# Kernel tuning notes

Hardware: AMD Instinct MI355X
Metric: run time of the kernel (lower is better)

Reference implementation:

```python
import jax, jax.numpy as jnp
import numpy as np

DIM = 768
GP_NUM = 49


def setup_inputs() -> dict:
    key = jax.random.key(0)
    ks = jax.random.split(key, 7)
    b, n, d = 16, 1024, DIM
    s = d ** -0.5
    x = jax.random.normal(ks[0], (b, n, d), dtype=jnp.float32)
    W_qkv = jax.random.normal(ks[1], (d, 3 * d), dtype=jnp.float32) * s
    b_qkv = jnp.zeros((3 * d,), dtype=jnp.float32)
    W_proj = jax.random.normal(ks[2], (d, d), dtype=jnp.float32) * s
    b_proj = jnp.zeros((d,), dtype=jnp.float32)
    W_gp = jax.random.normal(ks[3], (d, GP_NUM), dtype=jnp.float32) * s
    alpha = jnp.zeros((1,), dtype=jnp.float32)
    return {"x": x, "W_qkv": W_qkv, "b_qkv": b_qkv, "W_proj": W_proj,
            "b_proj": b_proj, "W_gp": W_gp, "alpha": alpha}


def reference(x, W_qkv, b_qkv, W_proj, b_proj, W_gp, alpha):
    d = x.shape[-1]
    scale = d ** -0.5
    qkv = x @ W_qkv + b_qkv                      # (b, n, 3d)
    q, k, v = jnp.split(qkv, 3, axis=-1)
    scores = jnp.einsum('bnd,bmd->bnm', q, k) * scale
    attn = jax.nn.softmax(scores, axis=-1)       # (b, n, n)
    gw = jax.nn.softmax(q @ W_gp, axis=-1)       # (b, n, gp_num)
    group = jnp.einsum('bng,bmg->bnm', gw, gw)   # (b, n, n)
    a = jax.nn.sigmoid(alpha)                    # (1,)
    weights = attn * (a + (1.0 - a) * group)
    out = jnp.einsum('bnm,bmd->bnd', weights, v)
    return out @ W_proj + b_proj
```

## Files before the change

### kernel.cpp

```cpp
#include <hip/hip_runtime.h>
#include <stdint.h>

typedef __attribute__((ext_vector_type(8))) short short8;
typedef __attribute__((ext_vector_type(4))) short short4v;
typedef __attribute__((ext_vector_type(4))) float floatx4;
typedef _Float16 half2v __attribute__((ext_vector_type(2)));

__device__ __forceinline__ float b2f(unsigned short u) {
  union { unsigned int i; float f; } v; v.i = ((unsigned int)u) << 16; return v.f;
}
__device__ __forceinline__ unsigned short f2b(float f) {
  union { float f; unsigned int i; } v; v.f = f;
  unsigned int i = v.i;
  return (unsigned short)((i + 0x7FFFu + ((i >> 16) & 1u)) >> 16);
}
__device__ __forceinline__ short4v pack4(float a, float b, float c, float d) {
  short4v r;
  r[0] = (short)f2b(a); r[1] = (short)f2b(b); r[2] = (short)f2b(c); r[3] = (short)f2b(d);
  return r;
}

__device__ __forceinline__ void stage16(const unsigned short* g, unsigned short* lds_base) {
  __builtin_amdgcn_global_load_lds((__attribute__((address_space(1))) const unsigned int*)g,
                                   (__attribute__((address_space(3))) unsigned int*)lds_base,
                                   16, 0, 0);
}

template<int SWZ>
__global__ __launch_bounds__(256, 4) void gemm_bt(
    const unsigned short* __restrict__ A, const unsigned short* __restrict__ B,
    unsigned short* __restrict__ Cb, float* __restrict__ Cf,
    const float* __restrict__ rowdiv, const float* __restrict__ bias,
    int K, int lda, int ldb, int ldc,
    long long sA, long long sB, long long sC, long long sRD)
{
  const int tid  = threadIdx.x;
  const int lane = tid & 63;
  const int wave = tid >> 6;
  const int wr = wave >> 1, wc = wave & 1;
  int m0, n0;
  if (SWZ) {
    const int lin  = blockIdx.x;
    const int xcd  = lin & 7;
    const int rem  = lin >> 3;
    const int yloc = rem / 18;
    const int x    = rem - yloc * 18;
    m0 = (xcd * 16 + yloc) * 128;
    n0 = x * 128;
  } else {
    m0 = blockIdx.y * 128;
    n0 = blockIdx.x * 128;
  }
  const int bz = blockIdx.z;
  A += (long long)bz * sA;
  B += (long long)bz * sB;
  const float* rd = rowdiv ? rowdiv + (long long)bz * sRD : (const float*)0;

  __shared__ unsigned short As[128 * 32];
  __shared__ unsigned short Bs[128 * 32];

  floatx4 acc[4][4];
#pragma unroll
  for (int i = 0; i < 4; ++i)
#pragma unroll
    for (int j = 0; j < 4; ++j) acc[i][j] = floatx4{0.f, 0.f, 0.f, 0.f};

  const int t    = (lane & 7) ^ (lane >> 3);
  const int srow = 2 * (lane >> 3) + (t >> 2);
  const int scol = (t & 3) * 8;
  const unsigned short* ga0 = A + (long long)(m0 + wave * 32 + srow) * lda + scol;
  const unsigned short* ga1 = ga0 + 16LL * lda;
  const unsigned short* gb0 = B + (long long)(n0 + wave * 32 + srow) * ldb + scol;
  const unsigned short* gb1 = gb0 + 16LL * ldb;
  unsigned short* lA0 = As + wave * 1024;
  unsigned short* lA1 = lA0 + 512;
  unsigned short* lB0 = Bs + wave * 1024;
  unsigned short* lB1 = lB0 + 512;

  const int l15  = lane & 15;
  const int q    = lane >> 4;
  const int rofs = (l15 >> 1) * 64 + (((q + 4 * (l15 & 1)) ^ (l15 >> 1)) * 8);

  for (int kt = 0; kt < K; kt += 32) {
    __syncthreads();
    stage16(ga0 + kt, lA0);
    stage16(ga1 + kt, lA1);
    stage16(gb0 + kt, lB0);
    stage16(gb1 + kt, lB1);
    __syncthreads();
    short8 af[4], bfv[4];
#pragma unroll
    for (int i = 0; i < 4; ++i) af[i]  = *(const short8*)&As[(wr * 32 + i * 8) * 64 + rofs];
#pragma unroll
    for (int j = 0; j < 4; ++j) bfv[j] = *(const short8*)&Bs[(wc * 32 + j * 8) * 64 + rofs];
#pragma unroll
    for (int i = 0; i < 4; ++i)
#pragma unroll
      for (int j = 0; j < 4; ++j)
        acc[i][j] = __builtin_amdgcn_mfma_f32_16x16x32_bf16(bfv[j], af[i], acc[i][j], 0, 0, 0);
  }

#pragma unroll
  for (int i = 0; i < 4; ++i) {
    const int row = m0 + wr * 64 + i * 16 + l15;
    const float rcp = rd ? __builtin_amdgcn_rcpf(rd[row]) : 1.0f;
#pragma unroll
    for (int j = 0; j < 4; ++j) {
      const int colb = n0 + wc * 64 + j * 16 + q * 4;
      floatx4 v = acc[i][j];
      if (rd) { v[0] *= rcp; v[1] *= rcp; v[2] *= rcp; v[3] *= rcp; }
      if (bias) {
        const float4 bi = *(const float4*)&bias[colb];
        v[0] += bi.x; v[1] += bi.y; v[2] += bi.z; v[3] += bi.w;
      }
      if (Cb) *(short4v*)&Cb[(long long)bz * sC + (long long)row * ldc + colb] = pack4(v[0], v[1], v[2], v[3]);
      else    *(floatx4*)&Cf[(long long)bz * sC + (long long)row * ldc + colb] = v;
    }
  }
}

__global__ __launch_bounds__(256) void score_weights(
    const unsigned short* __restrict__ qkv, const unsigned short* __restrict__ gw,
    unsigned short* __restrict__ Wout, float* __restrict__ L,
    const float* __restrict__ alpha)
{
  const int tid  = threadIdx.x;
  const int lane = tid & 63;
  const int wave = tid >> 6;
  const int wr = wave >> 1, wc = wave & 1;
  const int n0 = blockIdx.x * 128;
  const int m0 = blockIdx.y * 128;
  const int b  = blockIdx.z;

  const int l15 = lane & 15;
  const int q   = lane >> 4;
  const int q8  = q * 8;

  const unsigned short* gq = gw + ((long long)(b * 1024 + m0 + wr * 64)) * 64;
  const unsigned short* gk = gw + ((long long)(b * 1024 + n0 + wc * 64)) * 64;
  floatx4 gacc[4][4];
#pragma unroll
  for (int i = 0; i < 4; ++i)
#pragma unroll
    for (int j = 0; j < 4; ++j) gacc[i][j] = floatx4{0.f, 0.f, 0.f, 0.f};
#pragma unroll
  for (int ks = 0; ks < 2; ++ks) {
    short8 af[4], bfv[4];
#pragma unroll
    for (int i = 0; i < 4; ++i) af[i]  = *(const short8*)&gq[(long long)(i * 16 + l15) * 64 + ks * 32 + q8];
#pragma unroll
    for (int j = 0; j < 4; ++j) bfv[j] = *(const short8*)&gk[(long long)(j * 16 + l15) * 64 + ks * 32 + q8];
#pragma unroll
    for (int i = 0; i < 4; ++i)
#pragma unroll
      for (int j = 0; j < 4; ++j)
        gacc[i][j] = __builtin_amdgcn_mfma_f32_16x16x32_bf16(bfv[j], af[i], gacc[i][j], 0, 0, 0);
  }
  const float aa    = 1.0f / (1.0f + __expf(-alpha[0]));
  const float onema = 1.0f - aa;
  half2v gfp[4][4][2];
#pragma unroll
  for (int i = 0; i < 4; ++i)
#pragma unroll
    for (int j = 0; j < 4; ++j) {
      gfp[i][j][0] = half2v{(_Float16)(aa + onema * gacc[i][j][0]),
                            (_Float16)(aa + onema * gacc[i][j][1])};
      gfp[i][j][1] = half2v{(_Float16)(aa + onema * gacc[i][j][2]),
                            (_Float16)(aa + onema * gacc[i][j][3])};
    }

  const unsigned short* Aq = qkv + ((long long)(b * 1024 + m0)) * 2304;
  const unsigned short* Bk = qkv + ((long long)(b * 1024 + n0)) * 2304 + 768;

  __shared__ unsigned short As[128 * 32];
  __shared__ unsigned short Bs[128 * 32];

  floatx4 sacc[4][4];
#pragma unroll
  for (int i = 0; i < 4; ++i)
#pragma unroll
    for (int j = 0; j < 4; ++j) sacc[i][j] = floatx4{0.f, 0.f, 0.f, 0.f};

  const int t    = (lane & 7) ^ (lane >> 3);
  const int srow = 2 * (lane >> 3) + (t >> 2);
  const int scol = (t & 3) * 8;
  const unsigned short* ga0 = Aq + (long long)(wave * 32 + srow) * 2304 + scol;
  const unsigned short* ga1 = ga0 + 16LL * 2304;
  const unsigned short* gb0 = Bk + (long long)(wave * 32 + srow) * 2304 + scol;
  const unsigned short* gb1 = gb0 + 16LL * 2304;
  unsigned short* lA0 = As + wave * 1024;
  unsigned short* lA1 = lA0 + 512;
  unsigned short* lB0 = Bs + wave * 1024;
  unsigned short* lB1 = lB0 + 512;

  const int rofs = (l15 >> 1) * 64 + (((q + 4 * (l15 & 1)) ^ (l15 >> 1)) * 8);

  for (int kt = 0; kt < 768; kt += 32) {
    __syncthreads();
    stage16(ga0 + kt, lA0);
    stage16(ga1 + kt, lA1);
    stage16(gb0 + kt, lB0);
    stage16(gb1 + kt, lB1);
    __syncthreads();
    short8 af[4], bfv[4];
#pragma unroll
    for (int i = 0; i < 4; ++i) af[i]  = *(const short8*)&As[(wr * 32 + i * 8) * 64 + rofs];
#pragma unroll
    for (int j = 0; j < 4; ++j) bfv[j] = *(const short8*)&Bs[(wc * 32 + j * 8) * 64 + rofs];
#pragma unroll
    for (int i = 0; i < 4; ++i)
#pragma unroll
      for (int j = 0; j < 4; ++j)
        sacc[i][j] = __builtin_amdgcn_mfma_f32_16x16x32_bf16(bfv[j], af[i], sacc[i][j], 0, 0, 0);
  }

  const float scale = 0.03608439182435161f;
  unsigned short* Wb = Wout + ((long long)b << 20);

#pragma unroll
  for (int i = 0; i < 4; ++i) {
    const int row = m0 + wr * 64 + i * 16 + l15;
    float ls = 0.0f;
#pragma unroll
    for (int j = 0; j < 4; ++j) {
      const int colb = n0 + wc * 64 + j * 16 + q * 4;
      float e0 = __expf(sacc[i][j][0] * scale);
      float e1 = __expf(sacc[i][j][1] * scale);
      float e2 = __expf(sacc[i][j][2] * scale);
      float e3 = __expf(sacc[i][j][3] * scale);
      ls += (e0 + e1) + (e2 + e3);
      *(short4v*)&Wb[(long long)row * 1024 + colb] =
        pack4(e0 * (float)gfp[i][j][0][0], e1 * (float)gfp[i][j][0][1],
              e2 * (float)gfp[i][j][1][0], e3 * (float)gfp[i][j][1][1]);
    }
    ls += __shfl_xor(ls, 16, 64);
    ls += __shfl_xor(ls, 32, 64);
    if (lane < 16) atomicAdd(&L[b * 1024 + row], ls);
  }
}

__global__ __launch_bounds__(256) void gw_kernel(
    const unsigned short* __restrict__ qkv, const unsigned short* __restrict__ WgpT,
    unsigned short* __restrict__ gw)
{
  const int wave = threadIdx.x >> 6;
  const int lane = threadIdx.x & 63;
  const long long row = (long long)blockIdx.x * 4 + wave;
  const unsigned short* q = qkv + row * 2304;
  float qv[12];
#pragma unroll
  for (int j = 0; j < 12; ++j) qv[j] = b2f(q[lane + 64 * j]);

  float logit = -1e30f;
  for (int g = 0; g < 49; ++g) {
    const unsigned short* wg = WgpT + g * 768;
    float acc = 0.0f;
#pragma unroll
    for (int j = 0; j < 12; ++j) acc += qv[j] * b2f(wg[lane + 64 * j]);
#pragma unroll
    for (int m = 1; m < 64; m <<= 1) acc += __shfl_xor(acc, m, 64);
    if (lane == g) logit = acc;
  }
  float mx = logit;
#pragma unroll
  for (int m = 1; m < 64; m <<= 1) mx = fmaxf(mx, __shfl_xor(mx, m, 64));
  const float e = (lane < 49) ? __expf(logit - mx) : 0.0f;
  float s = e;
#pragma unroll
  for (int m = 1; m < 64; m <<= 1) s += __shfl_xor(s, m, 64);
  gw[row * 64 + lane] = f2b(e / s);
}

__global__ void convert_f2b(const float* __restrict__ in, unsigned short* __restrict__ out, long long n)
{
  long long i = ((long long)blockIdx.x * 256 + threadIdx.x) * 4;
  if (i + 3 >= n) {
    for (long long k = i; k < n; ++k) out[k] = f2b(in[k]);
    return;
  }
  float4 v = *(const float4*)(in + i);
  out[i + 0] = f2b(v.x);
  out[i + 1] = f2b(v.y);
  out[i + 2] = f2b(v.z);
  out[i + 3] = f2b(v.w);
}

__global__ void transpose_f2b(const float* __restrict__ in, unsigned short* __restrict__ out,
                              int R, int C, int ldin, int ldout)
{
  __shared__ unsigned short t[32][33];
  const int c0 = blockIdx.x * 32, r0 = blockIdx.y * 32;
  for (int i = threadIdx.y; i < 32; i += 8) {
    const int r = r0 + i, c = c0 + threadIdx.x;
    if (r < R && c < C) t[i][threadIdx.x] = f2b(in[(long long)r * ldin + c]);
  }
  __syncthreads();
  for (int i = threadIdx.y; i < 32; i += 8) {
    const int r = c0 + i, c = r0 + threadIdx.x;
    if (r < C && c < R) out[(long long)r * ldout + c] = t[threadIdx.x][i];
  }
}

extern "C" void kernel_launch(void* const* d_in, const int* in_sizes, int n_in,
                              void* d_out, int out_size, void* d_ws, size_t ws_size,
                              hipStream_t stream)
{
  const float* x      = (const float*)d_in[0];
  const float* W_qkv  = (const float*)d_in[1];
  const float* b_qkv  = (const float*)d_in[2];
  const float* W_proj = (const float*)d_in[3];
  const float* b_proj = (const float*)d_in[4];
  const float* W_gp   = (const float*)d_in[5];
  const float* alpha  = (const float*)d_in[6];

  char* p = (char*)d_ws;
  auto alloc = [&](size_t bytes) { char* r = p; p += (bytes + 255) & ~255ULL; return r; };
  unsigned short* qkv    = (unsigned short*)alloc(16384ULL * 2304 * 2);
  unsigned short* xb     = (unsigned short*)alloc(16384ULL * 768 * 2);
  unsigned short* WqkvT  = (unsigned short*)alloc(2304ULL * 768 * 2);
  unsigned short* WprojT = (unsigned short*)alloc(768ULL * 768 * 2);
  unsigned short* WgpT   = (unsigned short*)alloc(49ULL * 768 * 2);
  unsigned short* gwbuf  = (unsigned short*)alloc(16384ULL * 64 * 2);
  float*          Lbuf   = (float*)alloc(16384ULL * 4);
  unsigned short* wmat   = (unsigned short*)alloc(16ULL * 1024 * 1024 * 2);
  unsigned short* vpT    = (unsigned short*)alloc(16ULL * 768 * 1024 * 2);

  const dim3 blk256(256);
  const dim3 tb(32, 8);

  convert_f2b<<<dim3(12288), blk256, 0, stream>>>(x, xb, 16384LL * 768);
  transpose_f2b<<<dim3(72, 24), tb, 0, stream>>>(W_qkv, WqkvT, 768, 2304, 2304, 768);
  transpose_f2b<<<dim3(24, 24), tb, 0, stream>>>(W_proj, WprojT, 768, 768, 768, 768);
  transpose_f2b<<<dim3(2, 24), tb, 0, stream>>>(W_gp, WgpT, 768, 49, 49, 768);

  gemm_bt<1><<<dim3(2304, 1, 1), blk256, 0, stream>>>(xb, WqkvT, qkv, (float*)0,
                                                      (const float*)0, b_qkv,
                                                      768, 768, 768, 2304, 0, 0, 0, 0);

  gw_kernel<<<dim3(4096), blk256, 0, stream>>>(qkv, WgpT, gwbuf);

  hipMemsetAsync(Lbuf, 0, 16384 * 4, stream);

  score_weights<<<dim3(8, 8, 16), blk256, 0, stream>>>(qkv, gwbuf, wmat, Lbuf, alpha);

  gemm_bt<0><<<dim3(8, 6, 16), blk256, 0, stream>>>(WprojT, qkv + 1536, vpT, (float*)0,
                                                    (const float*)0, (const float*)0,
                                                    768, 768, 2304, 1024,
                                                    0, 1024LL * 2304, 768LL * 1024, 0);

  gemm_bt<0><<<dim3(6, 8, 16), blk256, 0, stream>>>(wmat, vpT, (unsigned short*)0, (float*)d_out,
                                                    Lbuf, b_proj,
                                                    1024, 1024, 1024, 768,
                                                    1024LL * 1024, 768LL * 1024, 1024LL * 768, 1024);
}
```

Baseline: 432.9 us.

## Replace 128x128 GEMM with 256x256 triple-buffered pipelined 8-wave kernel

The three bf16 GEMMs move from a 128x128 tile, 4-wave, single-buffered kernel to a 256x256 tile, 8-wave kernel. The new kernel triple-buffers LDS, prefetching two K-steps ahead with direct global-to-LDS loads, and interleaves half-tile MFMA blocks with the staging of the next tiles, using explicit waitcnt, sched barriers and setprio. The aim is to hide global-load latency and raise data reuse per block. In exchange it uses far more LDS and registers per block and launches fewer blocks, which can leave CUs underused on the smaller batched GEMMs.

```diff
diff --git a/kernel.cpp b/kernel.cpp
--- a/kernel.cpp
+++ b/kernel.cpp
@@ -27,7 +27,7 @@
 }
 
 template<int SWZ>
-__global__ __launch_bounds__(256, 4) void gemm_bt(
+__global__ __launch_bounds__(512, 2) void gemm256(
     const unsigned short* __restrict__ A, const unsigned short* __restrict__ B,
     unsigned short* __restrict__ Cb, float* __restrict__ Cf,
     const float* __restrict__ rowdiv, const float* __restrict__ bias,
@@ -37,31 +37,31 @@
   const int tid  = threadIdx.x;
   const int lane = tid & 63;
   const int wave = tid >> 6;
-  const int wr = wave >> 1, wc = wave & 1;
+  const int wr = wave >> 2;
+  const int wc = wave & 3;
   int m0, n0;
   if (SWZ) {
     const int lin  = blockIdx.x;
     const int xcd  = lin & 7;
     const int rem  = lin >> 3;
-    const int yloc = rem / 18;
-    const int x    = rem - yloc * 18;
-    m0 = (xcd * 16 + yloc) * 128;
-    n0 = x * 128;
+    const int yloc = rem / 9;
+    const int x    = rem - yloc * 9;
+    m0 = (xcd * 8 + yloc) * 256;
+    n0 = x * 256;
   } else {
-    m0 = blockIdx.y * 128;
-    n0 = blockIdx.x * 128;
+    m0 = blockIdx.y * 256;
+    n0 = blockIdx.x * 256;
   }
   const int bz = blockIdx.z;
   A += (long long)bz * sA;
   B += (long long)bz * sB;
   const float* rd = rowdiv ? rowdiv + (long long)bz * sRD : (const float*)0;
 
-  __shared__ unsigned short As[128 * 32];
-  __shared__ unsigned short Bs[128 * 32];
-
-  floatx4 acc[4][4];
-#pragma unroll
-  for (int i = 0; i < 4; ++i)
+  __shared__ __align__(16) unsigned short lds[3 * 16384];
+
+  floatx4 acc[8][4];
+#pragma unroll
+  for (int i = 0; i < 8; ++i)
 #pragma unroll
     for (int j = 0; j < 4; ++j) acc[i][j] = floatx4{0.f, 0.f, 0.f, 0.f};
 
@@ -72,37 +72,130 @@
   const unsigned short* ga1 = ga0 + 16LL * lda;
   const unsigned short* gb0 = B + (long long)(n0 + wave * 32 + srow) * ldb + scol;
   const unsigned short* gb1 = gb0 + 16LL * ldb;
-  unsigned short* lA0 = As + wave * 1024;
-  unsigned short* lA1 = lA0 + 512;
-  unsigned short* lB0 = Bs + wave * 1024;
-  unsigned short* lB1 = lB0 + 512;
 
   const int l15  = lane & 15;
   const int q    = lane >> 4;
   const int rofs = (l15 >> 1) * 64 + (((q + 4 * (l15 & 1)) ^ (l15 >> 1)) * 8);
 
-  for (int kt = 0; kt < K; kt += 32) {
-    __syncthreads();
-    stage16(ga0 + kt, lA0);
-    stage16(ga1 + kt, lA1);
-    stage16(gb0 + kt, lB0);
-    stage16(gb1 + kt, lB1);
-    __syncthreads();
-    short8 af[4], bfv[4];
-#pragma unroll
-    for (int i = 0; i < 4; ++i) af[i]  = *(const short8*)&As[(wr * 32 + i * 8) * 64 + rofs];
-#pragma unroll
-    for (int j = 0; j < 4; ++j) bfv[j] = *(const short8*)&Bs[(wc * 32 + j * 8) * 64 + rofs];
+  short8 af[4], bfv[4];
+
+  auto STAGE_A = [&](int kt, int buf) {
+    unsigned short* d = lds + buf * 16384 + wave * 1024;
+    stage16(ga0 + kt, d);
+    stage16(ga1 + kt, d + 512);
+  };
+  auto STAGE_B = [&](int kt, int buf) {
+    unsigned short* d = lds + buf * 16384 + 8192 + wave * 1024;
+    stage16(gb0 + kt, d);
+    stage16(gb1 + kt, d + 512);
+  };
+  auto READ_A = [&](int buf, int base) {
+    const unsigned short* Ab = lds + buf * 16384;
 #pragma unroll
     for (int i = 0; i < 4; ++i)
+      af[i] = *(const short8*)&Ab[(wr * 64 + (base + i) * 8) * 64 + rofs];
+  };
+  auto READ_B = [&](int buf) {
+    const unsigned short* Bb = lds + buf * 16384 + 8192;
+#pragma unroll
+    for (int j = 0; j < 4; ++j)
+      bfv[j] = *(const short8*)&Bb[(wc * 32 + j * 8) * 64 + rofs];
+  };
+  auto MFMA_BLK = [&](int h) {
+#pragma unroll
+    for (int i = 0; i < 4; ++i)
 #pragma unroll
       for (int j = 0; j < 4; ++j)
-        acc[i][j] = __builtin_amdgcn_mfma_f32_16x16x32_bf16(bfv[j], af[i], acc[i][j], 0, 0, 0);
-  }
-
-#pragma unroll
-  for (int i = 0; i < 4; ++i) {
-    const int row = m0 + wr * 64 + i * 16 + l15;
+        acc[h * 4 + i][j] = __builtin_amdgcn_mfma_f32_16x16x32_bf16(bfv[j], af[i], acc[h * 4 + i][j], 0, 0, 0);
+  };
+
+  const int nt = K >> 5;
+  int cur = 0;
+
+  STAGE_A(0, 0);  STAGE_B(0, 0);
+  STAGE_A(32, 1); STAGE_B(32, 1);
+  asm volatile("s_waitcnt vmcnt(4)" ::: "memory");
+  __builtin_amdgcn_sched_barrier(0);
+  __builtin_amdgcn_s_barrier();
+
+  for (int tt = 0; tt < nt - 2; ++tt) {
+    const int nb  = (cur == 0) ? 2 : cur - 1;
+    const int kt2 = (tt + 2) << 5;
+    READ_B(cur);
+    READ_A(cur, 0);
+    STAGE_A(kt2, nb);
+    __builtin_amdgcn_sched_barrier(0);
+    __builtin_amdgcn_s_barrier();
+    asm volatile("s_waitcnt lgkmcnt(0)" ::: "memory");
+    __builtin_amdgcn_sched_barrier(0);
+    __builtin_amdgcn_s_setprio(1);
+    MFMA_BLK(0);
+    __builtin_amdgcn_s_setprio(0);
+    __builtin_amdgcn_sched_barrier(0);
+    __builtin_amdgcn_s_barrier();
+    READ_A(cur, 4);
+    STAGE_B(kt2, nb);
+    __builtin_amdgcn_sched_barrier(0);
+    __builtin_amdgcn_s_barrier();
+    asm volatile("s_waitcnt lgkmcnt(0)" ::: "memory");
+    __builtin_amdgcn_sched_barrier(0);
+    __builtin_amdgcn_s_setprio(1);
+    MFMA_BLK(1);
+    __builtin_amdgcn_s_setprio(0);
+    asm volatile("s_waitcnt vmcnt(4)" ::: "memory");
+    __builtin_amdgcn_sched_barrier(0);
+    __builtin_amdgcn_s_barrier();
+    cur = (cur == 2) ? 0 : cur + 1;
+  }
+
+  {
+    READ_B(cur);
+    READ_A(cur, 0);
+    __builtin_amdgcn_sched_barrier(0);
+    __builtin_amdgcn_s_barrier();
+    asm volatile("s_waitcnt lgkmcnt(0)" ::: "memory");
+    __builtin_amdgcn_sched_barrier(0);
+    __builtin_amdgcn_s_setprio(1);
+    MFMA_BLK(0);
+    __builtin_amdgcn_s_setprio(0);
+    __builtin_amdgcn_sched_barrier(0);
+    __builtin_amdgcn_s_barrier();
+    READ_A(cur, 4);
+    __builtin_amdgcn_sched_barrier(0);
+    __builtin_amdgcn_s_barrier();
+    asm volatile("s_waitcnt lgkmcnt(0)" ::: "memory");
+    __builtin_amdgcn_sched_barrier(0);
+    __builtin_amdgcn_s_setprio(1);
+    MFMA_BLK(1);
+    __builtin_amdgcn_s_setprio(0);
+    asm volatile("s_waitcnt vmcnt(0)" ::: "memory");
+    __builtin_amdgcn_sched_barrier(0);
+    __builtin_amdgcn_s_barrier();
+    cur = (cur == 2) ? 0 : cur + 1;
+  }
+  {
+    READ_B(cur);
+    READ_A(cur, 0);
+    __builtin_amdgcn_sched_barrier(0);
+    __builtin_amdgcn_s_barrier();
+    asm volatile("s_waitcnt lgkmcnt(0)" ::: "memory");
+    __builtin_amdgcn_sched_barrier(0);
+    __builtin_amdgcn_s_setprio(1);
+    MFMA_BLK(0);
+    __builtin_amdgcn_s_setprio(0);
+    __builtin_amdgcn_sched_barrier(0);
+    __builtin_amdgcn_s_barrier();
+    READ_A(cur, 4);
+    asm volatile("s_waitcnt lgkmcnt(0)" ::: "memory");
+    __builtin_amdgcn_sched_barrier(0);
+    __builtin_amdgcn_s_setprio(1);
+    MFMA_BLK(1);
+    __builtin_amdgcn_s_setprio(0);
+  }
+
+#pragma unroll
+  for (int i = 0; i < 8; ++i) {
+    const int row = m0 + wr * 128 + i * 16 + l15;
     const float rcp = rd ? __builtin_amdgcn_rcpf(rd[row]) : 1.0f;
 #pragma unroll
     for (int j = 0; j < 4; ++j) {
@@ -326,6 +419,7 @@
   unsigned short* vpT    = (unsigned short*)alloc(16ULL * 768 * 1024 * 2);
 
   const dim3 blk256(256);
+  const dim3 blk512(512);
   const dim3 tb(32, 8);
 
   convert_f2b<<<dim3(12288), blk256, 0, stream>>>(x, xb, 16384LL * 768);
@@ -333,9 +427,9 @@
   transpose_f2b<<<dim3(24, 24), tb, 0, stream>>>(W_proj, WprojT, 768, 768, 768, 768);
   transpose_f2b<<<dim3(2, 24), tb, 0, stream>>>(W_gp, WgpT, 768, 49, 49, 768);
 
-  gemm_bt<1><<<dim3(2304, 1, 1), blk256, 0, stream>>>(xb, WqkvT, qkv, (float*)0,
-                                                      (const float*)0, b_qkv,
-                                                      768, 768, 768, 2304, 0, 0, 0, 0);
+  gemm256<1><<<dim3(576, 1, 1), blk512, 0, stream>>>(xb, WqkvT, qkv, (float*)0,
+                                                     (const float*)0, b_qkv,
+                                                     768, 768, 768, 2304, 0, 0, 0, 0);
 
   gw_kernel<<<dim3(4096), blk256, 0, stream>>>(qkv, WgpT, gwbuf);
 
@@ -343,12 +437,12 @@
 
   score_weights<<<dim3(8, 8, 16), blk256, 0, stream>>>(qkv, gwbuf, wmat, Lbuf, alpha);
 
-  gemm_bt<0><<<dim3(8, 6, 16), blk256, 0, stream>>>(WprojT, qkv + 1536, vpT, (float*)0,
+  gemm256<0><<<dim3(4, 3, 16), blk512, 0, stream>>>(WprojT, qkv + 1536, vpT, (float*)0,
                                                     (const float*)0, (const float*)0,
                                                     768, 768, 2304, 1024,
                                                     0, 1024LL * 2304, 768LL * 1024, 0);
 
-  gemm_bt<0><<<dim3(6, 8, 16), blk256, 0, stream>>>(wmat, vpT, (unsigned short*)0, (float*)d_out,
+  gemm256<0><<<dim3(3, 4, 16), blk512, 0, stream>>>(wmat, vpT, (unsigned short*)0, (float*)d_out,
                                                     Lbuf, b_proj,
                                                     1024, 1024, 1024, 768,
                                                     1024LL * 1024, 768LL * 1024, 1024LL * 768, 1024);
```

Result: no change. 437.6 us (+1.1%).

## Fold V projection into output projection weights and drop V from QKV GEMM

Applied to the files above, without the earlier changes.

Precomputes Wcomb = W_proj^T·W_v once per call so the V-times-W_proj GEMM works directly from x, removing the V third of the QKV GEMM and its stored output. The V bias is folded into a combined output bias, since the rows of the weight matrix sum to one only after normalisation by L. The gw logits are also moved to an MFMA kernel over zero-padded 64-column weights. This adds small weight-preprocessing kernels and extra bf16 rounding of the combined weights.

```diff
diff --git a/kernel.cpp b/kernel.cpp
--- a/kernel.cpp
+++ b/kernel.cpp
@@ -26,7 +26,7 @@
                                    16, 0, 0);
 }
 
-template<int SWZ>
+template<int SYT, int SXT>
 __global__ __launch_bounds__(256, 4) void gemm_bt(
     const unsigned short* __restrict__ A, const unsigned short* __restrict__ B,
     unsigned short* __restrict__ Cb, float* __restrict__ Cf,
@@ -39,13 +39,13 @@
   const int wave = tid >> 6;
   const int wr = wave >> 1, wc = wave & 1;
   int m0, n0;
-  if (SWZ) {
+  if constexpr (SYT > 0) {
     const int lin  = blockIdx.x;
     const int xcd  = lin & 7;
     const int rem  = lin >> 3;
-    const int yloc = rem / 18;
-    const int x    = rem - yloc * 18;
-    m0 = (xcd * 16 + yloc) * 128;
+    const int yloc = rem / SXT;
+    const int x    = rem - yloc * SXT;
+    m0 = (xcd * SYT + yloc) * 128;
     n0 = x * 128;
   } else {
     m0 = blockIdx.y * 128;
@@ -169,8 +169,8 @@
                             (_Float16)(aa + onema * gacc[i][j][3])};
     }
 
-  const unsigned short* Aq = qkv + ((long long)(b * 1024 + m0)) * 2304;
-  const unsigned short* Bk = qkv + ((long long)(b * 1024 + n0)) * 2304 + 768;
+  const unsigned short* Aq = qkv + ((long long)(b * 1024 + m0)) * 1536;
+  const unsigned short* Bk = qkv + ((long long)(b * 1024 + n0)) * 1536 + 768;
 
   __shared__ unsigned short As[128 * 32];
   __shared__ unsigned short Bs[128 * 32];
@@ -184,10 +184,10 @@
   const int t    = (lane & 7) ^ (lane >> 3);
   const int srow = 2 * (lane >> 3) + (t >> 2);
   const int scol = (t & 3) * 8;
-  const unsigned short* ga0 = Aq + (long long)(wave * 32 + srow) * 2304 + scol;
-  const unsigned short* ga1 = ga0 + 16LL * 2304;
-  const unsigned short* gb0 = Bk + (long long)(wave * 32 + srow) * 2304 + scol;
-  const unsigned short* gb1 = gb0 + 16LL * 2304;
+  const unsigned short* ga0 = Aq + (long long)(wave * 32 + srow) * 1536 + scol;
+  const unsigned short* ga1 = ga0 + 16LL * 1536;
+  const unsigned short* gb0 = Bk + (long long)(wave * 32 + srow) * 1536 + scol;
+  const unsigned short* gb1 = gb0 + 16LL * 1536;
   unsigned short* lA0 = As + wave * 1024;
   unsigned short* lA1 = lA0 + 512;
   unsigned short* lB0 = Bs + wave * 1024;
@@ -239,36 +239,97 @@
   }
 }
 
-__global__ __launch_bounds__(256) void gw_kernel(
-    const unsigned short* __restrict__ qkv, const unsigned short* __restrict__ WgpT,
+__global__ __launch_bounds__(256) void gw_mfma(
+    const unsigned short* __restrict__ qkv, const unsigned short* __restrict__ Wgp64,
     unsigned short* __restrict__ gw)
 {
+  const int lane = threadIdx.x & 63;
   const int wave = threadIdx.x >> 6;
+  const int l15  = lane & 15;
+  const int q    = lane >> 4;
+  const int q8   = q * 8;
+  const long long row0 = (long long)blockIdx.x * 64 + wave * 16;
+  const unsigned short* A = qkv + row0 * 1536;
+
+  floatx4 acc[4];
+#pragma unroll
+  for (int j = 0; j < 4; ++j) acc[j] = floatx4{0.f, 0.f, 0.f, 0.f};
+
+  for (int kt = 0; kt < 768; kt += 32) {
+    short8 af = *(const short8*)&A[(long long)l15 * 1536 + kt + q8];
+    short8 bf[4];
+#pragma unroll
+    for (int j = 0; j < 4; ++j)
+      bf[j] = *(const short8*)&Wgp64[(j * 16 + l15) * 768 + kt + q8];
+#pragma unroll
+    for (int j = 0; j < 4; ++j)
+      acc[j] = __builtin_amdgcn_mfma_f32_16x16x32_bf16(bf[j], af, acc[j], 0, 0, 0);
+  }
+
+  float mx = -1e30f;
+#pragma unroll
+  for (int j = 0; j < 4; ++j)
+#pragma unroll
+    for (int e = 0; e < 4; ++e) {
+      const int col = j * 16 + q * 4 + e;
+      if (col < 49) mx = fmaxf(mx, acc[j][e]);
+    }
+  mx = fmaxf(mx, __shfl_xor(mx, 16, 64));
+  mx = fmaxf(mx, __shfl_xor(mx, 32, 64));
+
+  float ev[4][4];
+  float s = 0.0f;
+#pragma unroll
+  for (int j = 0; j < 4; ++j)
+#pragma unroll
+    for (int e = 0; e < 4; ++e) {
+      const int col = j * 16 + q * 4 + e;
+      const float x = (col < 49) ? __expf(acc[j][e] - mx) : 0.0f;
+      ev[j][e] = x;
+      s += x;
+    }
+  s += __shfl_xor(s, 16, 64);
+  s += __shfl_xor(s, 32, 64);
+  const float inv = 1.0f / s;
+
+  unsigned short* out = gw + (row0 + l15) * 64;
+#pragma unroll
+  for (int j = 0; j < 4; ++j)
+    *(short4v*)&out[j * 16 + q * 4] =
+      pack4(ev[j][0] * inv, ev[j][1] * inv, ev[j][2] * inv, ev[j][3] * inv);
+}
+
+__global__ __launch_bounds__(256) void small_gemm_nt(
+    const unsigned short* __restrict__ A, const unsigned short* __restrict__ B,
+    unsigned short* __restrict__ C)
+{
   const int lane = threadIdx.x & 63;
-  const long long row = (long long)blockIdx.x * 4 + wave;
-  const unsigned short* q = qkv + row * 2304;
-  float qv[12];
-#pragma unroll
-  for (int j = 0; j < 12; ++j) qv[j] = b2f(q[lane + 64 * j]);
-
-  float logit = -1e30f;
-  for (int g = 0; g < 49; ++g) {
-    const unsigned short* wg = WgpT + g * 768;
-    float acc = 0.0f;
-#pragma unroll
-    for (int j = 0; j < 12; ++j) acc += qv[j] * b2f(wg[lane + 64 * j]);
-#pragma unroll
-    for (int m = 1; m < 64; m <<= 1) acc += __shfl_xor(acc, m, 64);
-    if (lane == g) logit = acc;
-  }
-  float mx = logit;
-#pragma unroll
-  for (int m = 1; m < 64; m <<= 1) mx = fmaxf(mx, __shfl_xor(mx, m, 64));
-  const float e = (lane < 49) ? __expf(logit - mx) : 0.0f;
-  float s = e;
-#pragma unroll
-  for (int m = 1; m < 64; m <<= 1) s += __shfl_xor(s, m, 64);
-  gw[row * 64 + lane] = f2b(e / s);
+  const int wave = threadIdx.x >> 6;
+  const int l15  = lane & 15;
+  const int q    = lane >> 4;
+  const int q8   = q * 8;
+  const int rows0 = (blockIdx.y * 4 + wave) * 16;
+  const int cols0 = blockIdx.x * 64;
+
+  floatx4 acc[4];
+#pragma unroll
+  for (int j = 0; j < 4; ++j) acc[j] = floatx4{0.f, 0.f, 0.f, 0.f};
+
+  for (int kt = 0; kt < 768; kt += 32) {
+    short8 af = *(const short8*)&A[(rows0 + l15) * 768 + kt + q8];
+    short8 bf[4];
+#pragma unroll
+    for (int j = 0; j < 4; ++j)
+      bf[j] = *(const short8*)&B[(cols0 + j * 16 + l15) * 768 + kt + q8];
+#pragma unroll
+    for (int j = 0; j < 4; ++j)
+      acc[j] = __builtin_amdgcn_mfma_f32_16x16x32_bf16(bf[j], af, acc[j], 0, 0, 0);
+  }
+
+  unsigned short* out = C + (rows0 + l15) * 768 + cols0;
+#pragma unroll
+  for (int j = 0; j < 4; ++j)
+    *(short4v*)&out[j * 16 + q * 4] = pack4(acc[j][0], acc[j][1], acc[j][2], acc[j][3]);
 }
 
 __global__ void convert_f2b(const float* __restrict__ in, unsigned short* __restrict__ out, long long n)
@@ -299,6 +360,31 @@
     const int r = c0 + i, c = r0 + threadIdx.x;
     if (r < C && c < R) out[(long long)r * ldout + c] = t[threadIdx.x][i];
   }
+}
+
+__global__ void slice_f2b(const float* __restrict__ in, unsigned short* __restrict__ out)
+{
+  const long long idx = (long long)blockIdx.x * 256 + threadIdx.x;
+  const int r = (int)(idx / 768), c = (int)(idx - (long long)r * 768);
+  out[idx] = f2b(in[(long long)r * 2304 + 1536 + c]);
+}
+
+__global__ __launch_bounds__(256) void bias2_kernel(
+    const unsigned short* __restrict__ WprojT, const float* __restrict__ b_qkv,
+    const float* __restrict__ b_proj, float* __restrict__ bias2)
+{
+  const int lane = threadIdx.x & 63;
+  const int wave = threadIdx.x >> 6;
+  const int j = blockIdx.x * 4 + wave;
+  float s = 0.0f;
+#pragma unroll
+  for (int tt = 0; tt < 12; ++tt) {
+    const int d = tt * 64 + lane;
+    s += b2f(WprojT[j * 768 + d]) * b_qkv[1536 + d];
+  }
+#pragma unroll
+  for (int m = 1; m < 64; m <<= 1) s += __shfl_xor(s, m, 64);
+  if (lane == 0) bias2[j] = b_proj[j] + s;
 }
 
 extern "C" void kernel_launch(void* const* d_in, const int* in_sizes, int n_in,
@@ -315,13 +401,16 @@
 
   char* p = (char*)d_ws;
   auto alloc = [&](size_t bytes) { char* r = p; p += (bytes + 255) & ~255ULL; return r; };
-  unsigned short* qkv    = (unsigned short*)alloc(16384ULL * 2304 * 2);
+  unsigned short* qk     = (unsigned short*)alloc(16384ULL * 1536 * 2);
   unsigned short* xb     = (unsigned short*)alloc(16384ULL * 768 * 2);
-  unsigned short* WqkvT  = (unsigned short*)alloc(2304ULL * 768 * 2);
+  unsigned short* WqkvT  = (unsigned short*)alloc(1536ULL * 768 * 2);
   unsigned short* WprojT = (unsigned short*)alloc(768ULL * 768 * 2);
-  unsigned short* WgpT   = (unsigned short*)alloc(49ULL * 768 * 2);
+  unsigned short* WvB    = (unsigned short*)alloc(768ULL * 768 * 2);
+  unsigned short* Wcomb  = (unsigned short*)alloc(768ULL * 768 * 2);
+  unsigned short* Wgp64  = (unsigned short*)alloc(64ULL * 768 * 2);
   unsigned short* gwbuf  = (unsigned short*)alloc(16384ULL * 64 * 2);
   float*          Lbuf   = (float*)alloc(16384ULL * 4);
+  float*          bias2  = (float*)alloc(768ULL * 4);
   unsigned short* wmat   = (unsigned short*)alloc(16ULL * 1024 * 1024 * 2);
   unsigned short* vpT    = (unsigned short*)alloc(16ULL * 768 * 1024 * 2);
 
@@ -329,27 +418,32 @@
   const dim3 tb(32, 8);
 
   convert_f2b<<<dim3(12288), blk256, 0, stream>>>(x, xb, 16384LL * 768);
-  transpose_f2b<<<dim3(72, 24), tb, 0, stream>>>(W_qkv, WqkvT, 768, 2304, 2304, 768);
+  transpose_f2b<<<dim3(48, 24), tb, 0, stream>>>(W_qkv, WqkvT, 768, 1536, 2304, 768);
   transpose_f2b<<<dim3(24, 24), tb, 0, stream>>>(W_proj, WprojT, 768, 768, 768, 768);
-  transpose_f2b<<<dim3(2, 24), tb, 0, stream>>>(W_gp, WgpT, 768, 49, 49, 768);
-
-  gemm_bt<1><<<dim3(2304, 1, 1), blk256, 0, stream>>>(xb, WqkvT, qkv, (float*)0,
-                                                      (const float*)0, b_qkv,
-                                                      768, 768, 768, 2304, 0, 0, 0, 0);
-
-  gw_kernel<<<dim3(4096), blk256, 0, stream>>>(qkv, WgpT, gwbuf);
+  hipMemsetAsync(Wgp64, 0, 64ULL * 768 * 2, stream);
+  transpose_f2b<<<dim3(2, 24), tb, 0, stream>>>(W_gp, Wgp64, 768, 49, 49, 768);
+  slice_f2b<<<dim3(2304), blk256, 0, stream>>>(W_qkv, WvB);
+
+  small_gemm_nt<<<dim3(12, 12), blk256, 0, stream>>>(WprojT, WvB, Wcomb);
+  bias2_kernel<<<dim3(192), blk256, 0, stream>>>(WprojT, b_qkv, b_proj, bias2);
+
+  gemm_bt<16, 12><<<dim3(1536, 1, 1), blk256, 0, stream>>>(xb, WqkvT, qk, (float*)0,
+                                                           (const float*)0, b_qkv,
+                                                           768, 768, 768, 1536, 0, 0, 0, 0);
+
+  gw_mfma<<<dim3(256), blk256, 0, stream>>>(qk, Wgp64, gwbuf);
 
   hipMemsetAsync(Lbuf, 0, 16384 * 4, stream);
 
-  score_weights<<<dim3(8, 8, 16), blk256, 0, stream>>>(qkv, gwbuf, wmat, Lbuf, alpha);
-
-  gemm_bt<0><<<dim3(8, 6, 16), blk256, 0, stream>>>(WprojT, qkv + 1536, vpT, (float*)0,
-                                                    (const float*)0, (const float*)0,
-                                                    768, 768, 2304, 1024,
-                                                    0, 1024LL * 2304, 768LL * 1024, 0);
-
-  gemm_bt<0><<<dim3(6, 8, 16), blk256, 0, stream>>>(wmat, vpT, (unsigned short*)0, (float*)d_out,
-                                                    Lbuf, b_proj,
-                                                    1024, 1024, 1024, 768,
-                                                    1024LL * 1024, 768LL * 1024, 1024LL * 768, 1024);
-}
+  score_weights<<<dim3(8, 8, 16), blk256, 0, stream>>>(qk, gwbuf, wmat, Lbuf, alpha);
+
+  gemm_bt<0, 0><<<dim3(8, 6, 16), blk256, 0, stream>>>(Wcomb, xb, vpT, (float*)0,
+                                                       (const float*)0, (const float*)0,
+                                                       768, 768, 768, 1024,
+                                                       0, 1024LL * 768, 768LL * 1024, 0);
+
+  gemm_bt<0, 0><<<dim3(6, 8, 16), blk256, 0, stream>>>(wmat, vpT, (unsigned short*)0, (float*)d_out,
+                                                       Lbuf, bias2,
+                                                       1024, 1024, 1024, 768,
+                                                       1024LL * 1024, 768LL * 1024, 1024LL * 768, 1024);
+}
```

After: 366.8 us. -15.3%, faster.
